# Optimization experiments

Hardware: AMD Instinct MI355X
Metric: run time of the kernel (lower is better)

The kernel has to match this reference:

```python
import jax, jax.numpy as jnp
import numpy as np

N_NODES = 50000
N_EDGES = 600000
C = 128
EC = 16
BN_EPS = 1e-5
ALPHA = 0.5


def setup_inputs() -> dict:
    key = jax.random.key(0)
    ks = jax.random.split(key, 8)
    x = jax.random.normal(ks[0], (N_NODES, C), dtype=jnp.float32)
    edge_index = jax.random.randint(ks[1], (2, N_EDGES), 0, N_NODES, dtype=jnp.int64)
    edge_attr = jax.random.normal(ks[2], (N_EDGES, EC), dtype=jnp.float32)
    return {
        "x": x,
        "edge_index": edge_index,
        "edge_attr": edge_attr,
        "bn_gamma": jnp.ones((C,), jnp.float32),
        "bn_beta": jnp.zeros((C,), jnp.float32),
        "edge_W": jax.random.normal(ks[3], (EC, C), dtype=jnp.float32) * 0.05,
        "conv_W": jax.random.normal(ks[4], (2, C, C), dtype=jnp.float32) * 0.05,
        "gru_w_ih": jax.random.normal(ks[5], (3 * C, C), dtype=jnp.float32) * 0.05,
        "gru_w_hh": jax.random.normal(ks[6], (3 * C, C), dtype=jnp.float32) * 0.05,
        "gru_b_ih": jnp.zeros((3 * C,), jnp.float32),
        "gru_b_hh": jnp.zeros((3 * C,), jnp.float32),
    }


def _gru_cell(m, h, w_ih, w_hh, b_ih, b_hh):
    # torch.nn.GRUCell math
    gi = m @ w_ih.T + b_ih          # [N, 3C]
    gh = h @ w_hh.T + b_hh          # [N, 3C]
    ir, iz, inn = jnp.split(gi, 3, axis=-1)
    hr, hz, hn = jnp.split(gh, 3, axis=-1)
    r = jax.nn.sigmoid(ir + hr)
    z = jax.nn.sigmoid(iz + hz)
    n = jnp.tanh(inn + r * hn)
    return (1.0 - z) * n + z * h


def reference(x, edge_index, edge_attr, bn_gamma, bn_beta, edge_W, conv_W,
              gru_w_ih, gru_w_hh, gru_b_ih, gru_b_hh):
    n = x.shape[0]
    # BatchNorm1d (training mode: batch statistics, biased variance)
    mean = jnp.mean(x, axis=0)
    var = jnp.var(x, axis=0)
    xh = (x - mean) * jax.lax.rsqrt(var + BN_EPS) * bn_gamma + bn_beta
    x0 = xh
    # edge feature projection (Linear, no bias)
    ea = edge_attr @ edge_W                       # [E, C]
    src, dst = edge_index[0], edge_index[1]
    deg = jax.ops.segment_sum(jnp.ones((src.shape[0], 1), xh.dtype), dst,
                              num_segments=n)
    deg = jnp.clip(deg, 1.0)                      # PyG 'mean' clamps count to 1
    h = xh
    for i in range(2):                            # GatedGraphConv num_layers=2
        m = h @ conv_W[i]                         # [N, C]
        msg = jax.nn.relu(m[src] + ea)            # gather + message
        agg = jax.ops.segment_sum(msg, dst, num_segments=n) / deg  # scatter-mean
        h = _gru_cell(agg, h, gru_w_ih, gru_w_hh, gru_b_ih, gru_b_hh)
    out = jax.nn.relu(h)
    return (1.0 - ALPHA) * out + ALPHA * x0       # residual, res_lin = Identity
```

## Files before the change

kernel.cpp:

```cpp
#include <hip/hip_runtime.h>

#define NN 50000
#define NN64 50048
#define NE 600000
#define CC 128

typedef float f32x4 __attribute__((ext_vector_type(4)));
typedef float f32x2 __attribute__((ext_vector_type(2)));
typedef short bf16x8 __attribute__((ext_vector_type(8)));
typedef unsigned short u16x4 __attribute__((ext_vector_type(4)));
typedef unsigned short u16x8 __attribute__((ext_vector_type(8)));
typedef _Float16 f16x2 __attribute__((ext_vector_type(2)));
typedef _Float16 f16x4 __attribute__((ext_vector_type(4)));
typedef _Float16 f16x8 __attribute__((ext_vector_type(8)));

#if defined(__has_builtin)
#if __has_builtin(__builtin_amdgcn_fdot2)
#define HAS_FDOT2 1
#endif
#endif

__device__ __forceinline__ unsigned short f2b(float f) {
  union { float f; unsigned int u; } c; c.f = f;
  unsigned int r = c.u + 0x7FFFu + ((c.u >> 16) & 1u);
  return (unsigned short)(r >> 16);
}
__device__ __forceinline__ void gload16(const unsigned short* g, unsigned short* l) {
  __builtin_amdgcn_global_load_lds((const __attribute__((address_space(1))) void*)g,
                                   (__attribute__((address_space(3))) void*)l, 16, 0, 0);
}

__global__ __launch_bounds__(256) void k_prep(const float* __restrict__ wih,
                                              const float* __restrict__ whh,
                                              const float* __restrict__ convW,
                                              const float* __restrict__ eW,
                                              unsigned short* __restrict__ wpack,
                                              unsigned short* __restrict__ cpack,
                                              f16x2* __restrict__ ewpk) {
  int i = blockIdx.x * 256 + threadIdx.x;
  if (i < 98304) {
    int k = i & 127, j = (i >> 7) & 127, half = (i >> 14) & 1, chunk = i >> 15;
    const float* srcm = half ? whh : wih;
    float v = srcm[(long)(chunk * 128 + j) * CC + k];
    wpack[(long)(((chunk * 2 + half) * 128 + j) << 7) + (k ^ ((j & 7) << 3))] = f2b(v);
  } else if (i < 131072) {
    int i2 = i - 98304;
    int k = i2 & 127, j = (i2 >> 7) & 127, layer = i2 >> 14;
    float v = convW[(long)(layer * 128 + k) * CC + j];
    cpack[(long)((layer * 128 + j) << 7) + (k ^ ((j & 7) << 3))] = f2b(v);
  } else if (i < 132096) {
    int i2 = i - 131072;
    int kp = i2 >> 7, ch = i2 & 127;
    f16x2 w; w.x = (_Float16)eW[(2 * kp) * CC + ch]; w.y = (_Float16)eW[(2 * kp + 1) * CC + ch];
    ewpk[i2] = w;
  }
}

__global__ __launch_bounds__(128) void k_bnstats(const float* __restrict__ x,
                                                 float* __restrict__ stats) {
  int c = threadIdx.x;
  float s = 0.f, s2 = 0.f;
  for (int r = blockIdx.x; r < NN; r += gridDim.x) {
    float v = x[(long)r * CC + c];
    s += v; s2 += v * v;
  }
  atomicAdd(&stats[c], s);
  atomicAdd(&stats[CC + c], s2);
}

__global__ __launch_bounds__(128) void k_bnfinal(float* __restrict__ stats,
                                                 const float* __restrict__ gamma,
                                                 const float* __restrict__ beta) {
  int c = threadIdx.x;
  float mean = stats[c] * (1.f / NN);
  float var = stats[CC + c] * (1.f / NN) - mean * mean;
  var = fmaxf(var, 0.f);
  float sc = gamma[c] * rsqrtf(var + 1e-5f);
  stats[2 * CC + c] = sc;
  stats[3 * CC + c] = beta[c] - mean * sc;
}

__global__ __launch_bounds__(256) void k_norm(const float* __restrict__ x,
                                              const float* __restrict__ stats,
                                              float* __restrict__ xh,
                                              unsigned short* __restrict__ xhb) {
  const int total4 = NN * CC / 4;
  for (int i = blockIdx.x * 256 + threadIdx.x; i < total4; i += gridDim.x * 256) {
    f32x4 v = ((const f32x4*)x)[i];
    int c4 = (i & 31) * 4;
    int r = i >> 5;
    f32x4 sc = *(const f32x4*)&stats[2 * CC + c4];
    f32x4 sh = *(const f32x4*)&stats[3 * CC + c4];
    v = v * sc + sh;
    ((f32x4*)xh)[i] = v;
    u16x4 b; b.x = f2b(v[0]); b.y = f2b(v[1]); b.z = f2b(v[2]); b.w = f2b(v[3]);
    *(u16x4*)&xhb[(long)r * CC + (c4 ^ ((r & 7) << 3))] = b;
  }
}

__global__ __launch_bounds__(256) void k_cnt(const int* __restrict__ dst, int* __restrict__ cnt) {
  for (int e = blockIdx.x * 256 + threadIdx.x; e < NE; e += gridDim.x * 256)
    atomicAdd(&cnt[dst[e]], 1);
}

__global__ __launch_bounds__(1024) void k_scan(const int* __restrict__ cnt, int* __restrict__ rowp) {
  __shared__ int part[1024];
  int t = threadIdx.x;
  const int CH = (NN + 1023) / 1024;
  int b = t * CH, e = b + CH; if (e > NN) e = NN; if (b > NN) b = NN;
  int s = 0;
  for (int i = b; i < e; ++i) s += cnt[i];
  part[t] = s;
  __syncthreads();
  for (int off = 1; off < 1024; off <<= 1) {
    int v = (t >= off) ? part[t - off] : 0;
    __syncthreads();
    part[t] += v;
    __syncthreads();
  }
  int excl = (t == 0) ? 0 : part[t - 1];
  for (int i = b; i < e; ++i) { rowp[i] = excl; excl += cnt[i]; }
  if (t == 1023) rowp[NN] = part[1023];
}

__global__ __launch_bounds__(256) void k_fill(const int* __restrict__ dst,
                                              const int* __restrict__ src,
                                              const float* __restrict__ eattr,
                                              const int* __restrict__ rowp,
                                              int* __restrict__ cursor,
                                              int* __restrict__ src_csr,
                                              _Float16* __restrict__ attr_csr) {
  for (int e = blockIdx.x * 256 + threadIdx.x; e < NE; e += gridDim.x * 256) {
    int d = dst[e];
    int pos = atomicAdd(&cursor[d], 1);
    int idx = rowp[d] + pos;
    src_csr[idx] = src[e];
    const f32x4* ar = (const f32x4*)(eattr + (long)e * 16);
    f32x4 a0 = ar[0], a1 = ar[1], a2 = ar[2], a3 = ar[3];
    f16x8 h0, h1;
#pragma unroll
    for (int q = 0; q < 4; ++q) { h0[q] = (_Float16)a0[q]; h0[4 + q] = (_Float16)a1[q]; }
#pragma unroll
    for (int q = 0; q < 4; ++q) { h1[q] = (_Float16)a2[q]; h1[4 + q] = (_Float16)a3[q]; }
    f16x8* orow = (f16x8*)&attr_csr[(long)idx * 16];
    orow[0] = h0; orow[1] = h1;
  }
}

__global__ __launch_bounds__(256) void k_mgemm(const unsigned short* __restrict__ Ab,
                                               const unsigned short* __restrict__ Bp,
                                               _Float16* __restrict__ O) {
  __shared__ __align__(16) unsigned short As[64 * 128];
  __shared__ __align__(16) unsigned short Bs[128 * 128];
  int tid = threadIdx.x;
  int blockRow = blockIdx.x * 64;
  const unsigned short* asrc = Ab + (long)blockRow * CC;
#pragma unroll
  for (int p = 0; p < 4; ++p) {
    int off8 = (p * 256 + tid) * 8;
    gload16(asrc + off8, As + off8);
  }
#pragma unroll
  for (int p = 0; p < 8; ++p) {
    int off8 = (p * 256 + tid) * 8;
    gload16(Bp + off8, Bs + off8);
  }
  __syncthreads();

  int wave = tid >> 6, lane = tid & 63;
  int rbase = wave * 16;
  int lrow = rbase + (lane & 15);
  int swz = (lane & 7) << 3;
  bf16x8 a[4];
#pragma unroll
  for (int ks = 0; ks < 4; ++ks)
    a[ks] = *(const bf16x8*)&As[lrow * 128 + ((ks * 32 + (lane >> 4) * 8) ^ swz)];

  f32x4 acc[8];
#pragma unroll
  for (int t = 0; t < 8; ++t) acc[t] = {0.f, 0.f, 0.f, 0.f};
#pragma unroll
  for (int t = 0; t < 8; ++t) {
    int col = t * 16 + (lane & 15);
#pragma unroll
    for (int ks = 0; ks < 4; ++ks) {
      bf16x8 bfr = *(const bf16x8*)&Bs[col * 128 + ((ks * 32 + (lane >> 4) * 8) ^ swz)];
      acc[t] = __builtin_amdgcn_mfma_f32_16x16x32_bf16(a[ks], bfr, acc[t], 0, 0, 0);
    }
  }
#pragma unroll
  for (int t = 0; t < 8; ++t) {
    int col = t * 16 + (lane & 15);
#pragma unroll
    for (int q = 0; q < 4; ++q) {
      int grow = blockRow + rbase + (lane >> 4) * 4 + q;
      if (grow < NN) O[(long)grow * CC + col] = (_Float16)acc[t][q];
    }
  }
}

__global__ __launch_bounds__(256) void k_agg(const _Float16* __restrict__ m,
                                             const _Float16* __restrict__ attr,
                                             const f16x2* __restrict__ ewpk,
                                             const int* __restrict__ src_csr,
                                             const int* __restrict__ rowp,
                                             unsigned short* __restrict__ agg) {
  int n = blockIdx.x * 4 + (threadIdx.x >> 6);
  int t = threadIdx.x & 63;
  f16x2 w0[8], w1[8];
#pragma unroll
  for (int kp = 0; kp < 8; ++kp) {
    f16x4 wv = *(const f16x4*)&ewpk[kp * 128 + 2 * t];
    w0[kp].x = wv.x; w0[kp].y = wv.y;
    w1[kp].x = wv.z; w1[kp].y = wv.w;
  }
  int b = rowp[n], e = rowp[n + 1];
  float acc0 = 0.f, acc1 = 0.f;
  union H8 { f16x8 v; f16x2 p[4]; };
#pragma unroll 2
  for (int i = b; i < e; ++i) {
    int s = src_csr[i];
    const f16x8* ap = (const f16x8*)(attr + (long)i * 16);
    H8 A0, A1; A0.v = ap[0]; A1.v = ap[1];
    f16x2 mp = *(const f16x2*)&m[(long)s * CC + 2 * t];
    float s0 = (float)mp.x, s1 = (float)mp.y;
#if HAS_FDOT2
#pragma unroll
    for (int kp = 0; kp < 4; ++kp) {
      s0 = __builtin_amdgcn_fdot2(A0.p[kp], w0[kp], s0, false);
      s1 = __builtin_amdgcn_fdot2(A0.p[kp], w1[kp], s1, false);
    }
#pragma unroll
    for (int kp = 0; kp < 4; ++kp) {
      s0 = __builtin_amdgcn_fdot2(A1.p[kp], w0[4 + kp], s0, false);
      s1 = __builtin_amdgcn_fdot2(A1.p[kp], w1[4 + kp], s1, false);
    }
#else
#pragma unroll
    for (int kp = 0; kp < 4; ++kp) {
      s0 = fmaf((float)A0.p[kp].x, (float)w0[kp].x, s0);
      s0 = fmaf((float)A0.p[kp].y, (float)w0[kp].y, s0);
      s1 = fmaf((float)A0.p[kp].x, (float)w1[kp].x, s1);
      s1 = fmaf((float)A0.p[kp].y, (float)w1[kp].y, s1);
    }
#pragma unroll
    for (int kp = 0; kp < 4; ++kp) {
      s0 = fmaf((float)A1.p[kp].x, (float)w0[4 + kp].x, s0);
      s0 = fmaf((float)A1.p[kp].y, (float)w0[4 + kp].y, s0);
      s1 = fmaf((float)A1.p[kp].x, (float)w1[4 + kp].x, s1);
      s1 = fmaf((float)A1.p[kp].y, (float)w1[4 + kp].y, s1);
    }
#endif
    acc0 += fmaxf(s0, 0.f);
    acc1 += fmaxf(s1, 0.f);
  }
  float d = (float)(e - b);
  if (d < 1.f) d = 1.f;
  float inv = 1.f / d;
  unsigned int o = (unsigned int)f2b(acc0 * inv) | ((unsigned int)f2b(acc1 * inv) << 16);
  int cidx = (2 * t) ^ ((n & 7) << 3);
  *(unsigned int*)&agg[(long)n * CC + cidx] = o;
}

__global__ __launch_bounds__(256) void k_gru(const unsigned short* __restrict__ aggb,
                                             const unsigned short* __restrict__ hb,
                                             const float* __restrict__ hin,
                                             const unsigned short* __restrict__ wpack,
                                             const float* __restrict__ bih,
                                             const float* __restrict__ bhh,
                                             float* __restrict__ hout,
                                             unsigned short* __restrict__ houtb,
                                             const float* __restrict__ resid) {
  __shared__ __align__(16) unsigned short Sa[32 * 128];
  __shared__ __align__(16) unsigned short Sh[32 * 128];
  __shared__ __align__(16) unsigned short Ws[2 * 128 * 128];
  int tid = threadIdx.x;
  int blockRow = blockIdx.x * 32;

  const unsigned short* sa_src = aggb + (long)blockRow * CC;
  const unsigned short* sh_src = hb + (long)blockRow * CC;
#pragma unroll
  for (int p = 0; p < 2; ++p) {
    int off8 = (p * 256 + tid) * 8;
    gload16(sa_src + off8, Sa + off8);
    gload16(sh_src + off8, Sh + off8);
  }
#pragma unroll
  for (int p = 0; p < 16; ++p) {
    int off8 = (p * 256 + tid) * 8;
    gload16(wpack + off8, Ws + off8);
  }
  __syncthreads();

  int wave = tid >> 6, lane = tid & 63;
  int r0 = (wave >> 1) * 16;
  int cb = (wave & 1) * 64;
  int lrow = r0 + (lane & 15);
  int swz = (lane & 7) << 3;
  bf16x8 aA[4], aH[4];
#pragma unroll
  for (int ks = 0; ks < 4; ++ks) {
    int off = lrow * 128 + ((ks * 32 + (lane >> 4) * 8) ^ swz);
    aA[ks] = *(const bf16x8*)&Sa[off];
    aH[ks] = *(const bf16x8*)&Sh[off];
  }

  float rg[4][4], zg[4][4];

#pragma unroll
  for (int chunk = 0; chunk < 3; ++chunk) {
    f32x4 gi[4], gh[4];
#pragma unroll
    for (int t = 0; t < 4; ++t) { gi[t] = {0.f, 0.f, 0.f, 0.f}; gh[t] = {0.f, 0.f, 0.f, 0.f}; }
#pragma unroll
    for (int t = 0; t < 4; ++t) {
      int col = cb + t * 16 + (lane & 15);
#pragma unroll
      for (int ks = 0; ks < 4; ++ks) {
        int wo = col * 128 + ((ks * 32 + (lane >> 4) * 8) ^ swz);
        bf16x8 bi_ = *(const bf16x8*)&Ws[wo];
        gi[t] = __builtin_amdgcn_mfma_f32_16x16x32_bf16(aA[ks], bi_, gi[t], 0, 0, 0);
        bf16x8 bh_ = *(const bf16x8*)&Ws[16384 + wo];
        gh[t] = __builtin_amdgcn_mfma_f32_16x16x32_bf16(aH[ks], bh_, gh[t], 0, 0, 0);
      }
    }
#pragma unroll
    for (int t = 0; t < 4; ++t) {
      int j = cb + t * 16 + (lane & 15);
      int jg = chunk * 128 + j;
      float bi = bih[jg], bh = bhh[jg];
#pragma unroll
      for (int q = 0; q < 4; ++q) {
        float giv = gi[t][q] + bi;
        float ghv = gh[t][q] + bh;
        if (chunk == 0) {
          rg[t][q] = 1.f / (1.f + __expf(-(giv + ghv)));
        } else if (chunk == 1) {
          zg[t][q] = 1.f / (1.f + __expf(-(giv + ghv)));
        } else {
          float nn = tanhf(giv + rg[t][q] * ghv);
          int grow = blockRow + r0 + (lane >> 4) * 4 + q;
          if (grow < NN) {
            long o = (long)grow * CC + j;
            float h = hin[o];
            float z = zg[t][q];
            float hv = (1.f - z) * nn + z * h;
            if (resid) {
              hout[o] = 0.5f * fmaxf(hv, 0.f) + 0.5f * resid[o];
            } else {
              hout[o] = hv;
              houtb[(long)grow * CC + (j ^ ((grow & 7) << 3))] = f2b(hv);
            }
          }
        }
      }
    }
    if (chunk < 2) {
      __syncthreads();
      const unsigned short* wsrc = wpack + (long)(chunk + 1) * 32768;
#pragma unroll
      for (int p = 0; p < 16; ++p) {
        int off8 = (p * 256 + tid) * 8;
        gload16(wsrc + off8, Ws + off8);
      }
      __syncthreads();
    }
  }
}

extern "C" void kernel_launch(void* const* d_in, const int* in_sizes, int n_in,
                              void* d_out, int out_size, void* d_ws, size_t ws_size,
                              hipStream_t stream) {
  const float* x     = (const float*)d_in[0];
  const int*   eidx  = (const int*)d_in[1];
  const float* eattr = (const float*)d_in[2];
  const float* gamma = (const float*)d_in[3];
  const float* beta  = (const float*)d_in[4];
  const float* eW    = (const float*)d_in[5];
  const float* convW = (const float*)d_in[6];
  const float* wih   = (const float*)d_in[7];
  const float* whh   = (const float*)d_in[8];
  const float* bih   = (const float*)d_in[9];
  const float* bhh   = (const float*)d_in[10];
  float* out = (float*)d_out;

  char* ws = (char*)d_ws;
  size_t off = 0;
  auto alloc = [&](size_t bytes) -> void* {
    void* p = ws + off;
    off += (bytes + 255) & ~(size_t)255;
    return p;
  };
  float* stats   = (float*)alloc(512 * 4);
  int*   cnt     = (int*)alloc((size_t)NN * 4);
  int*   cursor  = (int*)alloc((size_t)NN * 4);
  int*   rowp    = (int*)alloc((size_t)(NN + 1) * 4);
  int*   src_csr = (int*)alloc((size_t)NE * 4);
  _Float16* attr_csr = (_Float16*)alloc((size_t)NE * 16 * 2);
  float* xh      = (float*)alloc((size_t)NN * CC * 4);
  float* h1      = (float*)alloc((size_t)NN * CC * 4);
  unsigned short* xhb  = (unsigned short*)alloc((size_t)NN64 * CC * 2);
  unsigned short* h1b  = (unsigned short*)alloc((size_t)NN64 * CC * 2);
  _Float16* mb        = (_Float16*)alloc((size_t)NN64 * CC * 2);
  unsigned short* aggb = (unsigned short*)alloc((size_t)NN64 * CC * 2);
  unsigned short* wpack = (unsigned short*)alloc((size_t)98304 * 2);
  unsigned short* cpack = (unsigned short*)alloc((size_t)32768 * 2);
  f16x2* ewpk    = (f16x2*)alloc((size_t)1024 * 4);
  (void)ws_size;

  const int* srcv = eidx;
  const int* dstv = eidx + NE;

  hipMemsetAsync(stats, 0, 256 * 4, stream);
  hipMemsetAsync(cnt, 0, (size_t)NN * 4, stream);
  hipMemsetAsync(cursor, 0, (size_t)NN * 4, stream);

  k_prep<<<516, 256, 0, stream>>>(wih, whh, convW, eW, wpack, cpack, ewpk);
  k_bnstats<<<512, 128, 0, stream>>>(x, stats);
  k_bnfinal<<<1, 128, 0, stream>>>(stats, gamma, beta);
  k_norm<<<2048, 256, 0, stream>>>(x, stats, xh, xhb);

  k_cnt<<<1024, 256, 0, stream>>>(dstv, cnt);
  k_scan<<<1, 1024, 0, stream>>>(cnt, rowp);
  k_fill<<<1024, 256, 0, stream>>>(dstv, srcv, eattr, rowp, cursor, src_csr, attr_csr);

  k_mgemm<<<NN64 / 64, 256, 0, stream>>>(xhb, cpack, mb);
  k_agg<<<NN / 4, 256, 0, stream>>>(mb, attr_csr, ewpk, src_csr, rowp, aggb);
  k_gru<<<(NN + 31) / 32, 256, 0, stream>>>(aggb, xhb, xh, wpack, bih, bhh, h1, h1b, nullptr);

  k_mgemm<<<NN64 / 64, 256, 0, stream>>>(h1b, cpack + (size_t)128 * 128, mb);
  k_agg<<<NN / 4, 256, 0, stream>>>(mb, attr_csr, ewpk, src_csr, rowp, aggb);
  k_gru<<<(NN + 31) / 32, 256, 0, stream>>>(aggb, h1b, h1, wpack, bih, bhh, out, nullptr, xh);
}
```

Before: 577.7 us.

## Replace single-block prefix scan with three-phase multi-block scan

The CSR row-pointer scan ran in one 1024-thread block, where each thread serially walked a strided chunk of counts. It is now split into a per-block reduction, a single-block scan of the block sums, and a per-block local scan that adds the block offsets. This spreads the work across many CUs and makes the loads coalesced, at the cost of two extra kernel launches.

```diff
diff --git a/kernel.cpp b/kernel.cpp
--- a/kernel.cpp
+++ b/kernel.cpp
@@ -4,6 +4,7 @@
 #define NN64 50048
 #define NE 600000
 #define CC 128
+#define SCANB 196
 
 typedef float f32x4 __attribute__((ext_vector_type(4)));
 typedef float f32x2 __attribute__((ext_vector_type(2)));
@@ -103,24 +104,53 @@
     atomicAdd(&cnt[dst[e]], 1);
 }
 
-__global__ __launch_bounds__(1024) void k_scan(const int* __restrict__ cnt, int* __restrict__ rowp) {
-  __shared__ int part[1024];
+__global__ __launch_bounds__(256) void k_scan_a(const int* __restrict__ cnt,
+                                                int* __restrict__ blocksum) {
+  int t = threadIdx.x, b = blockIdx.x;
+  int idx = b * 256 + t;
+  int v = (idx < NN) ? cnt[idx] : 0;
+#pragma unroll
+  for (int off = 32; off; off >>= 1) v += __shfl_down(v, off, 64);
+  __shared__ int wsum[4];
+  if ((t & 63) == 0) wsum[t >> 6] = v;
+  __syncthreads();
+  if (t == 0) blocksum[b] = wsum[0] + wsum[1] + wsum[2] + wsum[3];
+}
+
+__global__ __launch_bounds__(256) void k_scan_b(const int* __restrict__ blocksum,
+                                                int* __restrict__ blockoff,
+                                                int* __restrict__ rowp) {
   int t = threadIdx.x;
-  const int CH = (NN + 1023) / 1024;
-  int b = t * CH, e = b + CH; if (e > NN) e = NN; if (b > NN) b = NN;
-  int s = 0;
-  for (int i = b; i < e; ++i) s += cnt[i];
-  part[t] = s;
+  int v = (t < SCANB) ? blocksum[t] : 0;
+  __shared__ int sd[256];
+  sd[t] = v;
   __syncthreads();
-  for (int off = 1; off < 1024; off <<= 1) {
-    int v = (t >= off) ? part[t - off] : 0;
+  for (int off = 1; off < 256; off <<= 1) {
+    int x = (t >= off) ? sd[t - off] : 0;
     __syncthreads();
-    part[t] += v;
+    sd[t] += x;
     __syncthreads();
   }
-  int excl = (t == 0) ? 0 : part[t - 1];
-  for (int i = b; i < e; ++i) { rowp[i] = excl; excl += cnt[i]; }
-  if (t == 1023) rowp[NN] = part[1023];
+  blockoff[t] = sd[t] - v;
+  if (t == 255) rowp[NN] = sd[255];
+}
+
+__global__ __launch_bounds__(256) void k_scan_c(const int* __restrict__ cnt,
+                                                const int* __restrict__ blockoff,
+                                                int* __restrict__ rowp) {
+  int t = threadIdx.x, b = blockIdx.x;
+  int idx = b * 256 + t;
+  int v = (idx < NN) ? cnt[idx] : 0;
+  __shared__ int sd[256];
+  sd[t] = v;
+  __syncthreads();
+  for (int off = 1; off < 256; off <<= 1) {
+    int x = (t >= off) ? sd[t - off] : 0;
+    __syncthreads();
+    sd[t] += x;
+    __syncthreads();
+  }
+  if (idx < NN) rowp[idx] = blockoff[b] + sd[t] - v;
 }
 
 __global__ __launch_bounds__(256) void k_fill(const int* __restrict__ dst,
@@ -395,6 +425,8 @@
   int*   cnt     = (int*)alloc((size_t)NN * 4);
   int*   cursor  = (int*)alloc((size_t)NN * 4);
   int*   rowp    = (int*)alloc((size_t)(NN + 1) * 4);
+  int*   blocksum = (int*)alloc(256 * 4);
+  int*   blockoff = (int*)alloc(256 * 4);
   int*   src_csr = (int*)alloc((size_t)NE * 4);
   _Float16* attr_csr = (_Float16*)alloc((size_t)NE * 16 * 2);
   float* xh      = (float*)alloc((size_t)NN * CC * 4);
@@ -421,7 +453,9 @@
   k_norm<<<2048, 256, 0, stream>>>(x, stats, xh, xhb);
 
   k_cnt<<<1024, 256, 0, stream>>>(dstv, cnt);
-  k_scan<<<1, 1024, 0, stream>>>(cnt, rowp);
+  k_scan_a<<<SCANB, 256, 0, stream>>>(cnt, blocksum);
+  k_scan_b<<<1, 256, 0, stream>>>(blocksum, blockoff, rowp);
+  k_scan_c<<<SCANB, 256, 0, stream>>>(cnt, blockoff, rowp);
   k_fill<<<1024, 256, 0, stream>>>(dstv, srcv, eattr, rowp, cursor, src_csr, attr_csr);
 
   k_mgemm<<<NN64 / 64, 256, 0, stream>>>(xhb, cpack, mb);
```

Result: faster. 509.6 us (-11.8%).
